# Optimization experiments

Hardware: AMD Instinct MI355X
Metric: run time of the kernel (lower is better)

## Reference

```python
import jax, jax.numpy as jnp
import numpy as np

N, D_IN, H, E, L = 8192, 512, 256, 262144, 2
LN_EPS = 1e-5


def _unique_edges(rng, n, e):
    # sample unique (src,tgt) pairs so scatter-set semantics are well-defined
    flat = np.unique(rng.integers(0, n * n, size=int(e * 1.2)))
    rng.shuffle(flat)
    flat = flat[:e]
    assert flat.shape[0] == e
    return np.stack([flat // n, flat % n]).astype(np.int64)


def setup_inputs() -> dict:
    key = jax.random.key(0)
    ks = jax.random.split(key, 8)
    rng = np.random.default_rng(0)
    inv = lambda fan: 1.0 / np.sqrt(fan)
    return {
        "node_features": jax.random.normal(ks[0], (N, D_IN), jnp.float32),
        "edge_index": jnp.asarray(_unique_edges(rng, N, E)),
        "W_in": jax.random.uniform(ks[1], (H, D_IN), jnp.float32, -inv(D_IN), inv(D_IN)),
        "b_in": jnp.zeros((H,), jnp.float32),
        "W_gat": jax.random.uniform(ks[2], (L, H, H), jnp.float32, -inv(H), inv(H)),
        "a_gat": jax.random.uniform(ks[3], (L, 2 * H), jnp.float32, -inv(2 * H), inv(2 * H)),
        "ln_g": jnp.ones((L, H), jnp.float32),
        "ln_b": jnp.zeros((L, H), jnp.float32),
        "W_pool": jax.random.uniform(ks[4], (1, H), jnp.float32, -inv(H), inv(H)),
        "b_pool": jnp.zeros((1,), jnp.float32),
    }


def _layer_norm(x, g, b):
    mu = x.mean(-1, keepdims=True)
    var = ((x - mu) ** 2).mean(-1, keepdims=True)
    return (x - mu) * jax.lax.rsqrt(var + LN_EPS) * g + b


def reference(node_features, edge_index, W_in, b_in, W_gat, a_gat, ln_g, ln_b, W_pool, b_pool):
    src, tgt = edge_index[0], edge_index[1]
    n = node_features.shape[0]
    h = node_features @ W_in.T + b_in  # (N, H)
    nl = W_gat.shape[0]
    for l in range(nl):
        hw = h @ W_gat[l].T  # (N, H)
        # attention score per edge: attn([h_src || h_tgt]) with LeakyReLU(0.2)
        e = hw[src] @ a_gat[l, :H] + hw[tgt] @ a_gat[l, H:]  # (E,)
        e = jnp.where(e > 0, e, 0.2 * e)
        # faithful to torch: dense NxN with zeros at non-edges, full-row softmax
        alpha = jnp.zeros((n, n), h.dtype).at[src, tgt].set(e)
        alpha = jax.nn.softmax(alpha, axis=-1)
        h_new = alpha @ hw  # (N, H)  (dropout is eval-mode identity)
        h = _layer_norm(h + h_new, ln_g[l], ln_b[l])
        h = jax.nn.elu(h)
    gate = jax.nn.sigmoid(h @ W_pool.T + b_pool)  # (N, 1)
    graph_emb = (gate * h).sum(axis=0)  # (H,)
    return h, graph_emb
```

## Files before the change

### kernel.cpp

```cpp
#include <hip/hip_runtime.h>
#include <hip/hip_bf16.h>
#include <stdint.h>
#include <math.h>

#define NN 8192
#define DIN 512
#define HH 256
#define EE 262144
#define CAP 96
#define LN_EPS 1e-5f

typedef __attribute__((ext_vector_type(8))) short bf16x8;
typedef __attribute__((ext_vector_type(4))) short s16x4;
typedef __attribute__((ext_vector_type(4))) float f32x4;
typedef __attribute__((ext_vector_type(2))) float f32x2;

#if defined(__has_builtin)
#if __has_builtin(__builtin_amdgcn_cvt_pk_f32_fp8) && __has_builtin(__builtin_amdgcn_cvt_pk_fp8_f32)
#define HAVE_FP8_CVT 1
#endif
#endif

__device__ __forceinline__ short f2bf_bits(float x) {
    __hip_bfloat16 b = __float2bfloat16(x);
    return __builtin_bit_cast(short, b);
}
__device__ __forceinline__ float bf2f(short s) {
    uint32_t u = ((uint32_t)(uint16_t)s) << 16;
    return __builtin_bit_cast(float, u);
}
__device__ __forceinline__ void load16_lds(const void* g, void* l) {
    __builtin_amdgcn_global_load_lds((const __attribute__((address_space(1))) uint32_t*)g,
                                     (__attribute__((address_space(3))) uint32_t*)l, 16, 0, 0);
}

__device__ __forceinline__ uint8_t f2fp8(float x) {
#ifdef HAVE_FP8_CVT
    uint32_t p = __builtin_amdgcn_cvt_pk_fp8_f32(x, 0.f, 0u, false);
    return (uint8_t)(p & 0xFF);
#else
    uint8_t s = (x < 0.f) ? 0x80 : 0;
    float a = fabsf(x);
    if (!(a == a)) return 0x7F;
    if (a >= 448.f) return s | 0x7E;
    if (a < 0.0009765625f) return s;
    int e; float mf = frexpf(a, &e);
    int E = e + 6;
    if (E <= 0) { int q = (int)(a * 512.f + 0.5f); if (q >= 8) return s | 0x08; return s | (uint8_t)q; }
    int q = (int)(mf * 16.f + 0.5f);
    if (q >= 16) { q = 8; E++; }
    if (E > 15 || (E == 15 && q - 8 > 6)) return s | 0x7E;
    return s | (uint8_t)((E << 3) | (q - 8));
#endif
}
__device__ __forceinline__ void fp8x4_to_f32(uint32_t w, float* f) {
#ifdef HAVE_FP8_CVT
    f32x2 a = __builtin_amdgcn_cvt_pk_f32_fp8(w, false);
    f32x2 b = __builtin_amdgcn_cvt_pk_f32_fp8(w, true);
    f[0] = a[0]; f[1] = a[1]; f[2] = b[0]; f[3] = b[1];
#else
#pragma unroll
    for (int i = 0; i < 4; i++) {
        uint8_t bb = (w >> (8 * i)) & 0xFF;
        int s = bb >> 7, e = (bb >> 3) & 15, m = bb & 7;
        float v = e ? ldexpf((float)(8 + m), e - 10) : ldexpf((float)m, -9);
        f[i] = s ? -v : v;
    }
#endif
}

#define NW1 (HH * DIN)
#define NW2 (2 * HH * HH)
#define NX (NN * DIN)
#define ZCOUNT (2 * (2 * NN + HH) + NN)
__global__ __launch_bounds__(256) void prep(const float* __restrict__ W_in, __hip_bfloat16* __restrict__ Wb_in,
                                            const float* __restrict__ W_gat, __hip_bfloat16* __restrict__ Wgb,
                                            const float* __restrict__ X, __hip_bfloat16* __restrict__ Xb,
                                            float* __restrict__ zbase, float* __restrict__ emb) {
    int gtid = blockIdx.x * 256 + threadIdx.x;
    if (gtid < ZCOUNT) ((int*)zbase)[gtid] = 0;
    if (gtid < HH) emb[gtid] = 0.f;
    int q = gtid * 4;
    const float* x;
    __hip_bfloat16* y;
    int b;
    if (q < NW1) { x = W_in; y = Wb_in; b = q; }
    else if (q < NW1 + NW2) { x = W_gat; y = Wgb; b = q - NW1; }
    else if (q < NW1 + NW2 + NX) { x = X; y = Xb; b = q - NW1 - NW2; }
    else return;
    float4 v = *(const float4*)(x + b);
    y[b + 0] = __float2bfloat16(v.x);
    y[b + 1] = __float2bfloat16(v.y);
    y[b + 2] = __float2bfloat16(v.z);
    y[b + 3] = __float2bfloat16(v.w);
}

__global__ void fill_buckets(const int* __restrict__ src, const int* __restrict__ tgt,
                             int* __restrict__ cnt, int* __restrict__ buck) {
    int k = (blockIdx.x * 256 + threadIdx.x) * 2;
    if (k < EE) {
        int2 sv = *(const int2*)(src + k);
        int2 tv = *(const int2*)(tgt + k);
        int p = atomicAdd(&cnt[sv.x], 1);
        if (p < CAP) buck[sv.x * CAP + p] = tv.x;
        p = atomicAdd(&cnt[sv.y], 1);
        if (p < CAP) buck[sv.y * CAP + p] = tv.y;
    }
}

__global__ __launch_bounds__(256) void gemm_bb_bias(const __hip_bfloat16* __restrict__ A,
                                                    const __hip_bfloat16* __restrict__ B,
                                                    const float* __restrict__ bias,
                                                    __hip_bfloat16* __restrict__ Cb,
                                                    int Nc, int K) {
    __shared__ __hip_bfloat16 As[64 * 32];
    __shared__ __hip_bfloat16 Bs[64 * 32];
    const int tid = threadIdx.x;
    const int row0 = blockIdx.y * 64, col0 = blockIdx.x * 64;
    const int w = tid >> 6, l = tid & 63;
    const int quad = l >> 4, r = l & 15;
    const int mh = (w & 1) * 32, nh = (w >> 1) * 32;
    f32x4 acc[2][2] = {};

    const int srow = tid >> 2, scol = (tid & 3) * 8;
    const __hip_bfloat16* gA = A + (size_t)(row0 + srow) * K + scol;
    const __hip_bfloat16* gB = B + (size_t)(col0 + srow) * K + scol;
    __hip_bfloat16* lA = &As[tid * 8];
    __hip_bfloat16* lB = &Bs[tid * 8];

    for (int k0 = 0; k0 < K; k0 += 32) {
        load16_lds(gA + k0, lA);
        load16_lds(gB + k0, lB);
        __syncthreads();
        bf16x8 aF[2], bF[2];
#pragma unroll
        for (int mi = 0; mi < 2; mi++)
            aF[mi] = *(const bf16x8*)&As[(mh + mi * 16 + r) * 32 + quad * 8];
#pragma unroll
        for (int ni = 0; ni < 2; ni++)
            bF[ni] = *(const bf16x8*)&Bs[(nh + ni * 16 + r) * 32 + quad * 8];
#pragma unroll
        for (int mi = 0; mi < 2; mi++)
#pragma unroll
            for (int ni = 0; ni < 2; ni++)
                acc[mi][ni] = __builtin_amdgcn_mfma_f32_16x16x32_bf16(aF[mi], bF[ni], acc[mi][ni], 0, 0, 0);
        __syncthreads();
    }

#pragma unroll
    for (int mi = 0; mi < 2; mi++)
#pragma unroll
        for (int ni = 0; ni < 2; ni++) {
            int gcol = col0 + nh + ni * 16 + r;
            float bv = bias[gcol];
#pragma unroll
            for (int reg = 0; reg < 4; reg++) {
                int grow = row0 + mh + mi * 16 + quad * 4 + reg;
                Cb[(size_t)grow * Nc + gcol] = __float2bfloat16(acc[mi][ni][reg] + bv);
            }
        }
}

__global__ __launch_bounds__(256) void gemm_bb_score(const __hip_bfloat16* __restrict__ A,
                                                     const __hip_bfloat16* __restrict__ B,
                                                     uint8_t* __restrict__ C8,
                                                     const float* __restrict__ ag1,
                                                     const float* __restrict__ ag2,
                                                     float* __restrict__ s1, float* __restrict__ s2,
                                                     float* __restrict__ St,
                                                     int Nc, int K) {
    __shared__ __hip_bfloat16 As[64 * 32];
    __shared__ __hip_bfloat16 Bs[64 * 32];
    const int tid = threadIdx.x;
    const int row0 = blockIdx.y * 64, col0 = blockIdx.x * 64;
    const int w = tid >> 6, l = tid & 63;
    const int quad = l >> 4, r = l & 15;
    const int mh = (w & 1) * 32, nh = (w >> 1) * 32;
    f32x4 acc[2][2] = {};

    const int srow = tid >> 2, scol = (tid & 3) * 8;
    const __hip_bfloat16* gA = A + (size_t)(row0 + srow) * K + scol;
    const __hip_bfloat16* gB = B + (size_t)(col0 + srow) * K + scol;
    __hip_bfloat16* lA = &As[tid * 8];
    __hip_bfloat16* lB = &Bs[tid * 8];

    for (int k0 = 0; k0 < K; k0 += 32) {
        load16_lds(gA + k0, lA);
        load16_lds(gB + k0, lB);
        __syncthreads();
        bf16x8 aF[2], bF[2];
#pragma unroll
        for (int mi = 0; mi < 2; mi++)
            aF[mi] = *(const bf16x8*)&As[(mh + mi * 16 + r) * 32 + quad * 8];
#pragma unroll
        for (int ni = 0; ni < 2; ni++)
            bF[ni] = *(const bf16x8*)&Bs[(nh + ni * 16 + r) * 32 + quad * 8];
#pragma unroll
        for (int mi = 0; mi < 2; mi++)
#pragma unroll
            for (int ni = 0; ni < 2; ni++)
                acc[mi][ni] = __builtin_amdgcn_mfma_f32_16x16x32_bf16(aF[mi], bF[ni], acc[mi][ni], 0, 0, 0);
        __syncthreads();
    }

#pragma unroll
    for (int mi = 0; mi < 2; mi++)
#pragma unroll
        for (int ni = 0; ni < 2; ni++) {
            int gcol = col0 + nh + ni * 16 + r;
#pragma unroll
            for (int reg = 0; reg < 4; reg++) {
                int grow = row0 + mh + mi * 16 + quad * 4 + reg;
                C8[(size_t)grow * Nc + gcol] = f2fp8(acc[mi][ni][reg]);
            }
        }

    float a1v[2], a2v[2];
#pragma unroll
    for (int ni = 0; ni < 2; ni++) {
        int gcol = col0 + nh + ni * 16 + r;
        a1v[ni] = ag1[gcol];
        a2v[ni] = ag2[gcol];
    }
#pragma unroll
    for (int mi = 0; mi < 2; mi++)
#pragma unroll
        for (int reg = 0; reg < 4; reg++) {
            float p1 = acc[mi][0][reg] * a1v[0] + acc[mi][1][reg] * a1v[1];
            float p2 = acc[mi][0][reg] * a2v[0] + acc[mi][1][reg] * a2v[1];
#pragma unroll
            for (int off = 1; off <= 8; off <<= 1) {
                p1 += __shfl_xor(p1, off);
                p2 += __shfl_xor(p2, off);
            }
            if (r == 0) {
                int grow = row0 + mh + mi * 16 + quad * 4 + reg;
                atomicAdd(&s1[grow], p1);
                atomicAdd(&s2[grow], p2);
            }
        }
#pragma unroll
    for (int ni = 0; ni < 2; ni++) {
        float pS = 0.f;
#pragma unroll
        for (int mi = 0; mi < 2; mi++)
#pragma unroll
            for (int reg = 0; reg < 4; reg++) pS += acc[mi][ni][reg];
        pS += __shfl_xor(pS, 16);
        pS += __shfl_xor(pS, 32);
        if (quad == 0) atomicAdd(&St[col0 + nh + ni * 16 + r], pS);
    }
}

__global__ __launch_bounds__(256) void gat_row(const __hip_bfloat16* __restrict__ hprev,
                                               const uint8_t* __restrict__ hw8,
                                               const int* __restrict__ cnt, const int* __restrict__ buck,
                                               const float* __restrict__ s1, const float* __restrict__ s2,
                                               const float* __restrict__ St,
                                               const float* __restrict__ lng, const float* __restrict__ lnb,
                                               const float* __restrict__ W_pool, const float* __restrict__ b_pool,
                                               float* __restrict__ houtf, __hip_bfloat16* __restrict__ houtb,
                                               float* __restrict__ gate, int last) {
    const int wv = threadIdx.x >> 6, lane = threadIdx.x & 63;
    const int half = lane >> 5, sl = lane & 31;
    const int i = blockIdx.x * 4 + wv;
    const int deg = min(cnt[i], CAP);
    const int base = i * CAP;
    const float s1i = s1[i];

    float u[8] = {};
    float lsum = 0.f;

    for (int kb = 0; kb < deg; kb += 64) {
        int k = kb + lane;
        float wk = 0.f;
        int ck = 0;
        if (k < deg) {
            int j = buck[base + k];
            float e = s1i + s2[j];
            e = e > 0.f ? e : 0.2f * e;
            wk = __expf(e) - 1.f;
            ck = j;
        }
        lsum += wk;
        int nb = min(64, deg - kb);
        int npair = (nb + 1) >> 1;
        for (int jj = 0; jj < npair; jj += 8) {
            int cj[8];
            float wj[8];
#pragma unroll
            for (int p = 0; p < 8; p++) {
                int e2 = 2 * (jj + p) + half;
                cj[p] = __shfl(ck, e2);
                wj[p] = __shfl(wk, e2);
            }
            uint2 hv[8];
#pragma unroll
            for (int p = 0; p < 8; p++)
                hv[p] = *(const uint2*)(hw8 + (size_t)cj[p] * HH + 8 * sl);
#pragma unroll
            for (int p = 0; p < 8; p++) {
                float f[8];
                fp8x4_to_f32(hv[p].x, f);
                fp8x4_to_f32(hv[p].y, f + 4);
#pragma unroll
                for (int q = 0; q < 8; q++) u[q] += wj[p] * f[q];
            }
        }
    }
#pragma unroll
    for (int q = 0; q < 8; q++) u[q] += __shfl_xor(u[q], 32);
#pragma unroll
    for (int off = 32; off; off >>= 1) lsum += __shfl_xor(lsum, off);
    const float inv = 1.f / ((float)NN + lsum);

    float4 Sa = *(const float4*)(St + 8 * sl);
    float4 Sb = *(const float4*)(St + 8 * sl + 4);
    float Sts[8] = { Sa.x, Sa.y, Sa.z, Sa.w, Sb.x, Sb.y, Sb.z, Sb.w };
    bf16x8 hp = *(const bf16x8*)((const short*)hprev + (size_t)i * HH + 8 * sl);
    float x[8];
    float part = 0.f;
#pragma unroll
    for (int q = 0; q < 8; q++) { x[q] = bf2f(hp[q]) + (Sts[q] + u[q]) * inv; part += x[q]; }
#pragma unroll
    for (int off = 16; off; off >>= 1) part += __shfl_xor(part, off);
    float mu = part * (1.f / HH);
    float d[8];
    float vs = 0.f;
#pragma unroll
    for (int q = 0; q < 8; q++) { d[q] = x[q] - mu; vs += d[q] * d[q]; }
#pragma unroll
    for (int off = 16; off; off >>= 1) vs += __shfl_xor(vs, off);
    float rstd = rsqrtf(vs * (1.f / HH) + LN_EPS);
    float4 ga = *(const float4*)(lng + 8 * sl);
    float4 gb = *(const float4*)(lng + 8 * sl + 4);
    float4 ba = *(const float4*)(lnb + 8 * sl);
    float4 bb = *(const float4*)(lnb + 8 * sl + 4);
    float gg[8] = { ga.x, ga.y, ga.z, ga.w, gb.x, gb.y, gb.z, gb.w };
    float bv[8] = { ba.x, ba.y, ba.z, ba.w, bb.x, bb.y, bb.z, bb.w };
    float y[8];
#pragma unroll
    for (int q = 0; q < 8; q++) {
        float t = d[q] * rstd * gg[q] + bv[q];
        y[q] = t > 0.f ? t : __expf(t) - 1.f;
    }

    const int co = 8 * sl + 4 * half;
    if (houtb) {
        s16x4 yv;
#pragma unroll
        for (int q = 0; q < 4; q++) yv[q] = f2bf_bits(y[4 * half + q]);
        *(s16x4*)((short*)houtb + (size_t)i * HH + co) = yv;
    }
    if (houtf) {
        float4 yf = { y[4 * half], y[4 * half + 1], y[4 * half + 2], y[4 * half + 3] };
        *(float4*)(houtf + (size_t)i * HH + co) = yf;
    }

    if (last) {
        float4 wa = *(const float4*)(W_pool + 8 * sl);
        float4 wb = *(const float4*)(W_pool + 8 * sl + 4);
        float wp[8] = { wa.x, wa.y, wa.z, wa.w, wb.x, wb.y, wb.z, wb.w };
        float p = 0.f;
#pragma unroll
        for (int q = 0; q < 8; q++) p += y[q] * wp[q];
#pragma unroll
        for (int off = 16; off; off >>= 1) p += __shfl_xor(p, off);
        if (lane == 0) gate[i] = 1.f / (1.f + __expf(-(p + b_pool[0])));
    }
}

__global__ __launch_bounds__(256) void pool_kernel(const float* __restrict__ h, const float* __restrict__ gate,
                                                   float* __restrict__ emb) {
    int c = threadIdx.x;
    int r0 = blockIdx.x * 32;
    float acc = 0.f;
#pragma unroll
    for (int rr = 0; rr < 32; rr++) {
        int r = r0 + rr;
        acc += gate[r] * h[(size_t)r * HH + c];
    }
    atomicAdd(&emb[c], acc);
}

extern "C" void kernel_launch(void* const* d_in, const int* in_sizes, int n_in,
                              void* d_out, int out_size, void* d_ws, size_t ws_size,
                              hipStream_t stream) {
    const float* X      = (const float*)d_in[0];
    const int*   ei     = (const int*)d_in[1];
    const float* W_in   = (const float*)d_in[2];
    const float* b_in   = (const float*)d_in[3];
    const float* W_gat  = (const float*)d_in[4];
    const float* a_gat  = (const float*)d_in[5];
    const float* ln_g   = (const float*)d_in[6];
    const float* ln_b   = (const float*)d_in[7];
    const float* W_pool = (const float*)d_in[8];
    const float* b_pool = (const float*)d_in[9];
    float* out = (float*)d_out;

    __hip_bfloat16* hb    = (__hip_bfloat16*)d_ws;
    uint8_t*        hw8   = (uint8_t*)(hb + (size_t)NN * HH);
    __hip_bfloat16* Wb_in = (__hip_bfloat16*)(hw8 + (size_t)NN * HH);
    __hip_bfloat16* Wgb   = Wb_in + (size_t)HH * DIN;
    __hip_bfloat16* Xb    = Wgb + (size_t)2 * HH * HH;
    float* zbase = (float*)(Xb + (size_t)NN * DIN);
    float* s1_0 = zbase;
    float* s2_0 = s1_0 + NN;
    float* St_0 = s2_0 + NN;
    float* s1_1 = St_0 + HH;
    float* s2_1 = s1_1 + NN;
    float* St_1 = s2_1 + NN;
    int* cnt  = (int*)(St_1 + HH);
    float* gate = (float*)(cnt + NN);
    int* buck = (int*)(gate + NN);

    const int* src = ei;
    const int* tgt = ei + EE;
    float* emb = out + (size_t)NN * HH;

    int prep_quads = (NW1 + NW2 + NX) / 4;
    prep<<<(prep_quads + 255) / 256, 256, 0, stream>>>(W_in, Wb_in, W_gat, Wgb, X, Xb, zbase, emb);

    fill_buckets<<<EE / 512, 256, 0, stream>>>(src, tgt, cnt, buck);

    gemm_bb_bias<<<dim3(HH / 64, NN / 64), 256, 0, stream>>>(Xb, Wb_in, b_in, hb, HH, DIN);

    for (int ll = 0; ll < 2; ll++) {
        float* s1 = ll ? s1_1 : s1_0;
        float* s2 = ll ? s2_1 : s2_0;
        float* St = ll ? St_1 : St_0;
        const float* ag = a_gat + (size_t)ll * 2 * HH;
        gemm_bb_score<<<dim3(HH / 64, NN / 64), 256, 0, stream>>>(hb, Wgb + (size_t)ll * HH * HH, hw8,
                                                                  ag, ag + HH, s1, s2, St, HH, HH);
        gat_row<<<NN / 4, 256, 0, stream>>>(hb, hw8, cnt, buck, s1, s2, St,
                                            ln_g + (size_t)ll * HH, ln_b + (size_t)ll * HH,
                                            W_pool, b_pool,
                                            (ll == 1) ? out : nullptr,
                                            (ll == 0) ? hb : nullptr,
                                            gate, ll);
    }

    pool_kernel<<<NN / 32, 256, 0, stream>>>(out, gate, emb);
}
```

Baseline: 171.4 us.

## Fuse input conversion and bucket fill into GEMM, fold pooling into GAT

Result: slower. 204.3 us (median of 2 runs) (+19.2%).

```diff
diff --git a/kernel.cpp b/kernel.cpp
--- a/kernel.cpp
+++ b/kernel.cpp
@@ -71,11 +71,9 @@
 
 #define NW1 (HH * DIN)
 #define NW2 (2 * HH * HH)
-#define NX (NN * DIN)
 #define ZCOUNT (2 * (2 * NN + HH) + NN)
 __global__ __launch_bounds__(256) void prep(const float* __restrict__ W_in, __hip_bfloat16* __restrict__ Wb_in,
                                             const float* __restrict__ W_gat, __hip_bfloat16* __restrict__ Wgb,
-                                            const float* __restrict__ X, __hip_bfloat16* __restrict__ Xb,
                                             float* __restrict__ zbase, float* __restrict__ emb) {
     int gtid = blockIdx.x * 256 + threadIdx.x;
     if (gtid < ZCOUNT) ((int*)zbase)[gtid] = 0;
@@ -85,52 +83,54 @@
     __hip_bfloat16* y;
     int b;
     if (q < NW1) { x = W_in; y = Wb_in; b = q; }
-    else if (q < NW1 + NW2) { x = W_gat; y = Wgb; b = q - NW1; }
-    else if (q < NW1 + NW2 + NX) { x = X; y = Xb; b = q - NW1 - NW2; }
-    else return;
+    else { x = W_gat; y = Wgb; b = q - NW1; }
     float4 v = *(const float4*)(x + b);
-    y[b + 0] = __float2bfloat16(v.x);
-    y[b + 1] = __float2bfloat16(v.y);
-    y[b + 2] = __float2bfloat16(v.z);
-    y[b + 3] = __float2bfloat16(v.w);
-}
-
-__global__ void fill_buckets(const int* __restrict__ src, const int* __restrict__ tgt,
-                             int* __restrict__ cnt, int* __restrict__ buck) {
-    int k = (blockIdx.x * 256 + threadIdx.x) * 2;
-    if (k < EE) {
+    s16x4 s = { f2bf_bits(v.x), f2bf_bits(v.y), f2bf_bits(v.z), f2bf_bits(v.w) };
+    *(s16x4*)((short*)y + b) = s;
+}
+
+#define GEMM_BLOCKS 512
+__global__ __launch_bounds__(256) void gemm_in_fill(const float* __restrict__ X,
+                                                    const __hip_bfloat16* __restrict__ B,
+                                                    const float* __restrict__ bias,
+                                                    __hip_bfloat16* __restrict__ Cb,
+                                                    const int* __restrict__ src, const int* __restrict__ tgt,
+                                                    int* __restrict__ cnt, int* __restrict__ buck) {
+    __shared__ __hip_bfloat16 As[64 * 32];
+    __shared__ __hip_bfloat16 Bs[64 * 32];
+    const int bid = blockIdx.x;
+    if (bid >= GEMM_BLOCKS) {
+        int k = ((bid - GEMM_BLOCKS) * 256 + threadIdx.x) * 2;
         int2 sv = *(const int2*)(src + k);
         int2 tv = *(const int2*)(tgt + k);
         int p = atomicAdd(&cnt[sv.x], 1);
         if (p < CAP) buck[sv.x * CAP + p] = tv.x;
         p = atomicAdd(&cnt[sv.y], 1);
         if (p < CAP) buck[sv.y * CAP + p] = tv.y;
-    }
-}
-
-__global__ __launch_bounds__(256) void gemm_bb_bias(const __hip_bfloat16* __restrict__ A,
-                                                    const __hip_bfloat16* __restrict__ B,
-                                                    const float* __restrict__ bias,
-                                                    __hip_bfloat16* __restrict__ Cb,
-                                                    int Nc, int K) {
-    __shared__ __hip_bfloat16 As[64 * 32];
-    __shared__ __hip_bfloat16 Bs[64 * 32];
+        return;
+    }
     const int tid = threadIdx.x;
-    const int row0 = blockIdx.y * 64, col0 = blockIdx.x * 64;
+    const int row0 = (bid >> 2) * 64, col0 = (bid & 3) * 64;
     const int w = tid >> 6, l = tid & 63;
     const int quad = l >> 4, r = l & 15;
     const int mh = (w & 1) * 32, nh = (w >> 1) * 32;
     f32x4 acc[2][2] = {};
 
     const int srow = tid >> 2, scol = (tid & 3) * 8;
-    const __hip_bfloat16* gA = A + (size_t)(row0 + srow) * K + scol;
-    const __hip_bfloat16* gB = B + (size_t)(col0 + srow) * K + scol;
-    __hip_bfloat16* lA = &As[tid * 8];
+    const float* gA = X + (size_t)(row0 + srow) * DIN + scol;
+    const __hip_bfloat16* gB = B + (size_t)(col0 + srow) * DIN + scol;
     __hip_bfloat16* lB = &Bs[tid * 8];
 
-    for (int k0 = 0; k0 < K; k0 += 32) {
-        load16_lds(gA + k0, lA);
+    for (int k0 = 0; k0 < DIN; k0 += 32) {
+        float4 a0 = *(const float4*)(gA + k0);
+        float4 a1 = *(const float4*)(gA + k0 + 4);
         load16_lds(gB + k0, lB);
+        bf16x8 av;
+        av[0] = f2bf_bits(a0.x); av[1] = f2bf_bits(a0.y);
+        av[2] = f2bf_bits(a0.z); av[3] = f2bf_bits(a0.w);
+        av[4] = f2bf_bits(a1.x); av[5] = f2bf_bits(a1.y);
+        av[6] = f2bf_bits(a1.z); av[7] = f2bf_bits(a1.w);
+        *(bf16x8*)&As[tid * 8] = av;
         __syncthreads();
         bf16x8 aF[2], bF[2];
 #pragma unroll
@@ -156,7 +156,7 @@
 #pragma unroll
             for (int reg = 0; reg < 4; reg++) {
                 int grow = row0 + mh + mi * 16 + quad * 4 + reg;
-                Cb[(size_t)grow * Nc + gcol] = __float2bfloat16(acc[mi][ni][reg] + bv);
+                Cb[(size_t)grow * HH + gcol] = __float2bfloat16(acc[mi][ni][reg] + bv);
             }
         }
 }
@@ -260,7 +260,8 @@
                                                const float* __restrict__ lng, const float* __restrict__ lnb,
                                                const float* __restrict__ W_pool, const float* __restrict__ b_pool,
                                                float* __restrict__ houtf, __hip_bfloat16* __restrict__ houtb,
-                                               float* __restrict__ gate, int last) {
+                                               float* __restrict__ emb, int last) {
+    __shared__ float emb_s[4][HH];
     const int wv = threadIdx.x >> 6, lane = threadIdx.x & 63;
     const int half = lane >> 5, sl = lane & 31;
     const int i = blockIdx.x * 4 + wv;
@@ -366,21 +367,14 @@
         for (int q = 0; q < 8; q++) p += y[q] * wp[q];
 #pragma unroll
         for (int off = 16; off; off >>= 1) p += __shfl_xor(p, off);
-        if (lane == 0) gate[i] = 1.f / (1.f + __expf(-(p + b_pool[0])));
-    }
-}
-
-__global__ __launch_bounds__(256) void pool_kernel(const float* __restrict__ h, const float* __restrict__ gate,
-                                                   float* __restrict__ emb) {
-    int c = threadIdx.x;
-    int r0 = blockIdx.x * 32;
-    float acc = 0.f;
-#pragma unroll
-    for (int rr = 0; rr < 32; rr++) {
-        int r = r0 + rr;
-        acc += gate[r] * h[(size_t)r * HH + c];
-    }
-    atomicAdd(&emb[c], acc);
+        float g = 1.f / (1.f + __expf(-(p + b_pool[0])));
+#pragma unroll
+        for (int q = 0; q < 4; q++) emb_s[wv][co + q] = g * y[4 * half + q];
+        __syncthreads();
+        int c = threadIdx.x;
+        float s = emb_s[0][c] + emb_s[1][c] + emb_s[2][c] + emb_s[3][c];
+        atomicAdd(&emb[c], s);
+    }
 }
 
 extern "C" void kernel_launch(void* const* d_in, const int* in_sizes, int n_in,
@@ -402,8 +396,7 @@
     uint8_t*        hw8   = (uint8_t*)(hb + (size_t)NN * HH);
     __hip_bfloat16* Wb_in = (__hip_bfloat16*)(hw8 + (size_t)NN * HH);
     __hip_bfloat16* Wgb   = Wb_in + (size_t)HH * DIN;
-    __hip_bfloat16* Xb    = Wgb + (size_t)2 * HH * HH;
-    float* zbase = (float*)(Xb + (size_t)NN * DIN);
+    float* zbase = (float*)(Wgb + (size_t)2 * HH * HH);
     float* s1_0 = zbase;
     float* s2_0 = s1_0 + NN;
     float* St_0 = s2_0 + NN;
@@ -411,19 +404,15 @@
     float* s2_1 = s1_1 + NN;
     float* St_1 = s2_1 + NN;
     int* cnt  = (int*)(St_1 + HH);
-    float* gate = (float*)(cnt + NN);
-    int* buck = (int*)(gate + NN);
+    int* buck = (int*)(cnt + NN);
 
     const int* src = ei;
     const int* tgt = ei + EE;
     float* emb = out + (size_t)NN * HH;
 
-    int prep_quads = (NW1 + NW2 + NX) / 4;
-    prep<<<(prep_quads + 255) / 256, 256, 0, stream>>>(W_in, Wb_in, W_gat, Wgb, X, Xb, zbase, emb);
-
-    fill_buckets<<<EE / 512, 256, 0, stream>>>(src, tgt, cnt, buck);
-
-    gemm_bb_bias<<<dim3(HH / 64, NN / 64), 256, 0, stream>>>(Xb, Wb_in, b_in, hb, HH, DIN);
+    prep<<<256, 256, 0, stream>>>(W_in, Wb_in, W_gat, Wgb, zbase, emb);
+
+    gemm_in_fill<<<GEMM_BLOCKS + EE / 512, 256, 0, stream>>>(X, Wb_in, b_in, hb, src, tgt, cnt, buck);
 
     for (int ll = 0; ll < 2; ll++) {
         float* s1 = ll ? s1_1 : s1_0;
@@ -437,8 +426,6 @@
                                             W_pool, b_pool,
                                             (ll == 1) ? out : nullptr,
                                             (ll == 0) ? hb : nullptr,
-                                            gate, ll);
-    }
-
-    pool_kernel<<<NN / 32, 256, 0, stream>>>(out, gate, emb);
-}
+                                            emb, ll);
+    }
+}
```
